# Kernel tuning notes

Hardware: AMD Instinct MI355X
Metric: run time of the kernel (lower is better)

The kernel has to match this reference:

```python
import jax, jax.numpy as jnp
import numpy as np

G = 8        # n_games
D_IN = 128   # per-game state dim
A = 16       # per-game action dim
H1 = 600     # n_hidden_1
H2 = 500     # n_hidden_2
B = 32768    # batch


def setup_inputs() -> dict:
    key = jax.random.key(0)
    ks = jax.random.split(key, 12)
    u = lambda k, shape, bound: jax.random.uniform(k, shape, jnp.float32, -bound, bound)
    state = jax.random.normal(ks[0], (B, D_IN), jnp.float32)
    action = jax.random.normal(ks[1], (B, A), jnp.float32)
    idx = jnp.sort(jax.random.randint(ks[2], (B,), 0, G)).astype(jnp.int32)
    inp = {
        "state": state,
        "action": action,
        "idx": idx,
        # per-game first layer: Linear(D_IN -> H1), uniform(-1/sqrt(fan_in))
        "W1": u(ks[3], (G, H1, D_IN), 1.0 / np.sqrt(D_IN)),
        "b1": u(ks[4], (G, H1), 1.0 / np.sqrt(D_IN)),
        # shared state layer: Linear(H1 -> H2)
        "W2s": u(ks[5], (H2, H1), 1.0 / np.sqrt(H1)),
        "b2s": u(ks[6], (H2,), 1.0 / np.sqrt(H1)),
        # per-game action layer: Linear(A -> H2, bias=False)
        "W2a": u(ks[7], (G, H2, A), 1.0 / np.sqrt(A)),
        # per-game output head: Linear(H2 -> 1), uniform(-0.003, 0.003)
        "W3": u(ks[8], (G, H2), 0.003),
        "b3": u(ks[9], (G,), 0.003),
    }
    return inp


def reference(state, action, idx, W1, b1, W2s, b2s, W2a, W3, b3):
    # Per-game h1 for all games, then pick the routed game per sample.
    # (Reference-clean equivalent of the Python loop over unique idx; idx is
    #  sorted so the original's group reordering is the identity.)
    h1_all = jax.nn.relu(jnp.einsum('bd,ghd->bgh', state, W1) + b1)      # [B,G,H1]
    h1 = jnp.take_along_axis(h1_all, idx[:, None, None], axis=1)[:, 0]  # [B,H1]

    h2a_all = jnp.einsum('ba,gha->bgh', action, W2a)                     # [B,G,H2]
    h2a = jnp.take_along_axis(h2a_all, idx[:, None, None], axis=1)[:, 0]

    h2 = jnp.einsum('bh,kh->bk', h1, W2s) + b2s + h2a                    # [B,H2]
    h_f = jax.nn.relu(h2)  # features == 'relu'

    q_all = jnp.einsum('bh,gh->bg', h_f, W3) + b3                        # [B,G]
    q = jnp.take_along_axis(q_all, idx[:, None], axis=1)[:, 0]           # [B]
    return q
```

## Files before the change

### kernel.cpp

```cpp
#include <hip/hip_runtime.h>

#define G_ 8
#define DIN 128
#define ACT 16
#define H1 600
#define H2 500
#define H1P 608
#define H2P 512
#define BT 128
#define NBLK 256
#define NCHUNK 19
#define NTHR 512

#define OFF_W2S 0
#define OFF_W1  622592
#define OFF_W2A 1867776
#define OFF_B1  1998848
#define OFF_B2S 2018304
#define OFF_W3  2020352
#define PREP_BYTES 2036736

#define LDS_H1  0u
#define LDS_W1  16384u
#define LDS_B1  32768u
#define LDS_IDX 52224u
#define LDS_RED 52736u
#define LDS_TOTAL 56832

typedef __attribute__((ext_vector_type(8))) short short8;
typedef __attribute__((ext_vector_type(4))) float f32x4;
typedef __attribute__((ext_vector_type(16))) float f32x16;

__device__ __forceinline__ unsigned short f2bf(float f) {
  unsigned u = __float_as_uint(f);
  unsigned r = u + 0x7fffu + ((u >> 16) & 1u);
  return (unsigned short)(r >> 16);
}

__device__ __forceinline__ short8 pack8(const float* v) {
  short8 p;
#pragma unroll
  for (int j = 0; j < 8; ++j) p[j] = (short)f2bf(v[j]);
  return p;
}

__device__ __forceinline__ unsigned long long pack4(f32x4 v) {
  unsigned long long pk = 0;
#pragma unroll
  for (int j = 0; j < 4; ++j)
    pk |= (unsigned long long)f2bf(v[j]) << (16 * j);
  return pk;
}

__device__ __forceinline__ void stage1k(unsigned lds_off, const void* g) {
  __builtin_amdgcn_global_load_lds(
      (const __attribute__((address_space(1))) unsigned int*)(unsigned long long)g,
      (__attribute__((address_space(3))) unsigned int*)lds_off,
      16, 0, 0);
}

__global__ __launch_bounds__(256) void prep_kernel(
    const float* __restrict__ W1, const float* __restrict__ b1,
    const float* __restrict__ W2s, const float* __restrict__ b2s,
    const float* __restrict__ W2a, const float* __restrict__ W3,
    char* __restrict__ ws)
{
  unsigned long long* w2s_img = (unsigned long long*)(ws + OFF_W2S);
  unsigned long long* w1_img  = (unsigned long long*)(ws + OFF_W1);
  unsigned long long* w2a_img = (unsigned long long*)(ws + OFF_W2A);
  float* b1p  = (float*)(ws + OFF_B1);
  float* b2sp = (float*)(ws + OFF_B2S);
  float* w3p  = (float*)(ws + OFF_W3);
  const int tid = blockIdx.x * blockDim.x + threadIdx.x;
  const int nthr = gridDim.x * blockDim.x;

  for (int u = tid; u < 75000; u += nthr) {
    const int e0 = u * 4;
    const int c = e0 / 600, k0 = e0 - c * 600;
    f32x4 v = *(const f32x4*)(W2s + e0);
    const int chunk = k0 >> 5, t = (k0 >> 4) & 1, khi = (k0 >> 3) & 1, j0 = k0 & 7;
    const int l = (c & 31) + khi * 32, ct = c >> 5;
    const int base = ((chunk * 2 + t) * 16 + ct) * 64 + l;
    w2s_img[base * 2 + (j0 >> 2)] = pack4(v);
  }
  for (int u = tid; u < 153600; u += nthr) {
    const int e0 = u * 4;
    const int g = e0 / 76800;
    const int rem = e0 - g * 76800;
    const int f = rem >> 7, d0 = rem & 127;
    f32x4 v = *(const f32x4*)(W1 + e0);
    const int chunk = f >> 5, ft = (f >> 4) & 1, fl = f & 15;
    const int ks = d0 >> 5, lhi = (d0 >> 3) & 3, j0 = d0 & 7;
    const int base = ((g * NCHUNK + chunk) * 8 + ks * 2 + ft) * 64 + (lhi * 16 + fl);
    w1_img[base * 2 + (j0 >> 2)] = pack4(v);
  }
  for (int u = tid; u < 16000; u += nthr) {
    const int e0 = u * 4;
    const int g = e0 / 8000;
    const int rem = e0 - g * 8000;
    const int c = rem >> 4, a0 = rem & 15;
    f32x4 v = *(const f32x4*)(W2a + e0);
    const int khi = (a0 >> 3) & 1, j0 = a0 & 7;
    const int l = (c & 31) + khi * 32, ct = c >> 5;
    const int base = (g * 16 + ct) * 64 + l;
    w2a_img[base * 2 + (j0 >> 2)] = pack4(v);
  }
  for (int e = tid; e < G_ * H1; e += nthr) {
    const int g = e / H1, f = e - g * H1;
    b1p[g * H1P + f] = b1[e];
  }
  for (int e = tid; e < H2; e += nthr) b2sp[e] = b2s[e];
  for (int e = tid; e < G_ * H2; e += nthr) {
    const int g = e / H2, c = e - g * H2;
    w3p[g * H2P + c] = W3[e];
  }
}

__global__ __launch_bounds__(NTHR, 2) void critic_fused(
    const float* __restrict__ state, const float* __restrict__ action,
    const int* __restrict__ idx, const float* __restrict__ b3,
    const char* __restrict__ ws, float* __restrict__ out)
{
  extern __shared__ char smem[];
  const int tid = threadIdx.x, lane = tid & 63, w = tid >> 6;
  const int s0 = blockIdx.x * BT;
  int* idx_lds = (int*)(smem + LDS_IDX);
  float* b1lds = (float*)(smem + LDS_B1);
  float* red   = (float*)(smem + LDS_RED);

  const unsigned short* w2simg = (const unsigned short*)(ws + OFF_W2S);
  const unsigned short* w1img  = (const unsigned short*)(ws + OFF_W1);
  const unsigned short* w2aimg = (const unsigned short*)(ws + OFF_W2A);
  const float* b1p  = (const float*)(ws + OFF_B1);
  const float* b2sp = (const float*)(ws + OFF_B2S);
  const float* w3p  = (const float*)(ws + OFF_W3);

  if (tid < BT) idx_lds[tid] = idx[s0 + tid];
  for (int u = tid; u < (G_ * H1P) / 4; u += NTHR)
    ((f32x4*)b1lds)[u] = ((const f32x4*)b1p)[u];
  __syncthreads();
  const int g_lo = idx_lds[0], g_hi = idx_lds[BT - 1];
  const int myg  = idx_lds[w * 16 + (lane & 15)];

  short8 bs[4];
  {
    const float* sp = state + (size_t)(s0 + w * 16 + (lane & 15)) * DIN + ((lane >> 4) << 3);
#pragma unroll
    for (int ks = 0; ks < 4; ++ks) {
      float v[8];
      f32x4 t0 = *(const f32x4*)(sp + ks * 32), t1 = *(const f32x4*)(sp + ks * 32 + 4);
      v[0]=t0[0];v[1]=t0[1];v[2]=t0[2];v[3]=t0[3];
      v[4]=t1[0];v[5]=t1[1];v[6]=t1[2];v[7]=t1[3];
      bs[ks] = pack8(v);
    }
  }
  short8 bact[4];
#pragma unroll
  for (int nt = 0; nt < 4; ++nt) {
    const float* ap = action + (size_t)(s0 + nt * 32 + (lane & 31)) * ACT + ((lane >> 5) << 3);
    float v[8];
    f32x4 a0 = *(const f32x4*)ap, a1 = *(const f32x4*)(ap + 4);
    v[0]=a0[0];v[1]=a0[1];v[2]=a0[2];v[3]=a0[3];
    v[4]=a1[0];v[5]=a1[1];v[6]=a1[2];v[7]=a1[3];
    bact[nt] = pack8(v);
  }

  const char* w1src = (const char*)(ws + OFF_W1) + (size_t)g_lo * NCHUNK * 8192;
  stage1k(LDS_W1 + (unsigned)(tid * 16), w1src + tid * 16);
  stage1k(LDS_W1 + (unsigned)(8192 + tid * 16), w1src + 8192 + tid * 16);

  short8 afc[2][2], afn[2][2];
#pragma unroll
  for (int t = 0; t < 2; ++t)
#pragma unroll
    for (int cti = 0; cti < 2; ++cti)
      afc[t][cti] = *(const short8*)(w2simg + ((((size_t)0 * 2 + t) * 16 + w * 2 + cti) * 64 + lane) * 8);

  f32x16 acc[2][4];
#pragma unroll
  for (int a = 0; a < 2; ++a)
#pragma unroll
    for (int n = 0; n < 4; ++n)
#pragma unroll
      for (int r = 0; r < 16; ++r) acc[a][n][r] = 0.f;
  for (int g = g_lo; g <= g_hi; ++g) {
#pragma unroll
    for (int cti = 0; cti < 2; ++cti) {
      short8 af = *(const short8*)(w2aimg + (((size_t)g * 16 + w * 2 + cti) * 64 + lane) * 8);
#pragma unroll
      for (int nt = 0; nt < 4; ++nt) {
        f32x16 z;
#pragma unroll
        for (int r = 0; r < 16; ++r) z[r] = 0.f;
        f32x16 t = __builtin_amdgcn_mfma_f32_32x32x16_bf16(af, bact[nt], z, 0, 0, 0);
        const bool p = (idx_lds[nt * 32 + (lane & 31)] == g);
#pragma unroll
        for (int r = 0; r < 16; ++r) acc[cti][nt][r] = p ? t[r] : acc[cti][nt][r];
      }
    }
  }

  auto produce = [&](int c, int buf) {
    f32x4 kept[2];
#pragma unroll
    for (int f = 0; f < 2; ++f) { kept[f][0]=0.f;kept[f][1]=0.f;kept[f][2]=0.f;kept[f][3]=0.f; }
    for (int g = g_lo; g <= g_hi; ++g) {
      f32x4 a1[2];
#pragma unroll
      for (int f = 0; f < 2; ++f) { a1[f][0]=0.f;a1[f][1]=0.f;a1[f][2]=0.f;a1[f][3]=0.f; }
#pragma unroll
      for (int ks = 0; ks < 4; ++ks)
#pragma unroll
        for (int ft = 0; ft < 2; ++ft) {
          short8 aw;
          if (g == g_lo)
            aw = *(const short8*)(smem + LDS_W1 + (unsigned)(buf * 8192 + ((ks * 2 + ft) * 64 + lane) * 16));
          else
            aw = *(const short8*)(w1img + (((size_t)(g * NCHUNK + c) * 8 + ks * 2 + ft) * 64 + lane) * 8);
          a1[ft] = __builtin_amdgcn_mfma_f32_16x16x32_bf16(aw, bs[ks], a1[ft], 0, 0, 0);
        }
      if (myg == g) { kept[0] = a1[0]; kept[1] = a1[1]; }
    }
    const int kloc = (lane >> 4) << 2, khalf = lane >> 5;
    const int nt = w >> 1, s32 = (w & 1) * 16 + (lane & 15);
#pragma unroll
    for (int ft = 0; ft < 2; ++ft) {
      const int f0 = c * 32 + ft * 16 + kloc;
      f32x4 bv = *(const f32x4*)(b1lds + myg * H1P + f0);
      unsigned long long pk = 0;
#pragma unroll
      for (int r = 0; r < 4; ++r) {
        float hv = fmaxf(kept[ft][r] + bv[r], 0.f);
        pk |= (unsigned long long)f2bf(hv) << (16 * r);
      }
      *(unsigned long long*)(smem + LDS_H1 + (unsigned)(buf * 8192 +
          (ft * 4 + nt) * 1024 + (khalf * 32 + s32) * 16 + (kloc & 7) * 2)) = pk;
    }
  };

  asm volatile("s_waitcnt vmcnt(0)" ::: "memory");
  __builtin_amdgcn_sched_barrier(0);
  produce(0, 0);
  asm volatile("s_waitcnt lgkmcnt(0)" ::: "memory");
  __builtin_amdgcn_sched_barrier(0);
  __builtin_amdgcn_s_barrier();

  for (int i = 0; i < NCHUNK; ++i) {
    const int cur = i & 1;
    if (i + 2 < NCHUNK)
      stage1k(LDS_W1 + (unsigned)(cur * 8192 + tid * 16),
              w1src + (size_t)(i + 2) * 8192 + tid * 16);
    if (i + 1 < NCHUNK) {
#pragma unroll
      for (int t = 0; t < 2; ++t)
#pragma unroll
        for (int cti = 0; cti < 2; ++cti)
          afn[t][cti] = *(const short8*)(w2simg + ((((size_t)(i + 1) * 2 + t) * 16 + w * 2 + cti) * 64 + lane) * 8);
    }
    short8 bf[2][4];
#pragma unroll
    for (int t = 0; t < 2; ++t)
#pragma unroll
      for (int nt = 0; nt < 4; ++nt)
        bf[t][nt] = *(const short8*)(smem + LDS_H1 + (unsigned)(cur * 8192 + ((t * 4 + nt) * 64 + lane) * 16));
    __builtin_amdgcn_s_setprio(1);
#pragma unroll
    for (int t = 0; t < 2; ++t)
#pragma unroll
      for (int cti = 0; cti < 2; ++cti)
#pragma unroll
        for (int nt = 0; nt < 4; ++nt)
          acc[cti][nt] = __builtin_amdgcn_mfma_f32_32x32x16_bf16(afc[t][cti], bf[t][nt], acc[cti][nt], 0, 0, 0);
    __builtin_amdgcn_s_setprio(0);
    if (i + 1 < NCHUNK) {
      if (i + 2 < NCHUNK) { asm volatile("s_waitcnt vmcnt(5)" ::: "memory"); }
      else                { asm volatile("s_waitcnt vmcnt(4)" ::: "memory"); }
      __builtin_amdgcn_sched_barrier(0);
      produce(i + 1, cur ^ 1);
    }
    asm volatile("s_waitcnt lgkmcnt(0)" ::: "memory");
    __builtin_amdgcn_sched_barrier(0);
    __builtin_amdgcn_s_barrier();
#pragma unroll
    for (int t = 0; t < 2; ++t)
#pragma unroll
      for (int cti = 0; cti < 2; ++cti)
        afc[t][cti] = afn[t][cti];
  }

  float qp[4] = {0.f, 0.f, 0.f, 0.f};
  int gs[4];
#pragma unroll
  for (int nt = 0; nt < 4; ++nt) gs[nt] = idx_lds[nt * 32 + (lane & 31)];
#pragma unroll
  for (int cti = 0; cti < 2; ++cti) {
    const int cbase = (w * 2 + cti) * 32 + ((lane >> 5) << 2);
#pragma unroll
    for (int r = 0; r < 16; ++r) {
      const int c = cbase + (r & 3) + ((r >> 2) << 3);
      const float b2v = b2sp[c];
#pragma unroll
      for (int nt = 0; nt < 4; ++nt) {
        float v2 = fmaxf(acc[cti][nt][r] + b2v, 0.f);
        qp[nt] += v2 * w3p[gs[nt] * H2P + c];
      }
    }
  }
#pragma unroll
  for (int nt = 0; nt < 4; ++nt) {
    float v = qp[nt] + __shfl_xor(qp[nt], 32, 64);
    if (lane < 32) red[w * BT + nt * 32 + lane] = v;
  }
  __syncthreads();
  if (tid < BT) {
    float s = 0.f;
#pragma unroll
    for (int ww = 0; ww < 8; ++ww) s += red[ww * BT + tid];
    out[s0 + tid] = s + b3[idx_lds[tid]];
  }
}

extern "C" void kernel_launch(void* const* d_in, const int* in_sizes, int n_in,
                              void* d_out, int out_size, void* d_ws, size_t ws_size,
                              hipStream_t stream) {
  const float* state  = (const float*)d_in[0];
  const float* action = (const float*)d_in[1];
  const int*   idx    = (const int*)d_in[2];
  const float* W1     = (const float*)d_in[3];
  const float* b1     = (const float*)d_in[4];
  const float* W2s    = (const float*)d_in[5];
  const float* b2s    = (const float*)d_in[6];
  const float* W2a    = (const float*)d_in[7];
  const float* W3     = (const float*)d_in[8];
  const float* b3     = (const float*)d_in[9];
  float* out = (float*)d_out;
  char* ws = (char*)d_ws;

  hipMemsetAsync(ws, 0, PREP_BYTES, stream);
  hipLaunchKernelGGL(prep_kernel, dim3(1024), dim3(256), 0, stream,
                     W1, b1, W2s, b2s, W2a, W3, ws);
  hipLaunchKernelGGL(critic_fused, dim3(NBLK), dim3(NTHR), LDS_TOTAL, stream,
                     state, action, idx, b3, ws, out);
}
```

Measured before the change: 126.3 us.

## Deepen W1 LDS pipeline to four chunks, stage both game sides, drop memset

Rewrites the main loop to process two chunks per phase. It uses a four-deep ring of W1 and h1 LDS buffers, and stages W1 for both the low and high game into LDS instead of reading the second game straight from global memory. The prep kernel now writes zero padding itself, which removes the hipMemsetAsync, and b1 is staged into LDS asynchronously. LDS use grows to about 125 KB, which likely allows only one block per CU instead of the two declared in launch bounds. The chunk-pairing index logic near the tail looks delicate.

```diff
diff --git a/kernel.cpp b/kernel.cpp
--- a/kernel.cpp
+++ b/kernel.cpp
@@ -5,27 +5,27 @@
 #define ACT 16
 #define H1 600
 #define H2 500
-#define H1P 608
 #define H2P 512
+#define B1S 768
 #define BT 128
 #define NBLK 256
 #define NCHUNK 19
+#define NPHASE 9
 #define NTHR 512
 
 #define OFF_W2S 0
 #define OFF_W1  622592
 #define OFF_W2A 1867776
 #define OFF_B1  1998848
-#define OFF_B2S 2018304
-#define OFF_W3  2020352
-#define PREP_BYTES 2036736
+#define OFF_B2S 2023424
+#define OFF_W3  2025472
 
 #define LDS_H1  0u
-#define LDS_W1  16384u
-#define LDS_B1  32768u
-#define LDS_IDX 52224u
-#define LDS_RED 52736u
-#define LDS_TOTAL 56832
+#define LDS_W1  32768u
+#define LDS_B1  98304u
+#define LDS_IDX 122880u
+#define LDS_RED 123392u
+#define LDS_TOTAL 127488
 
 typedef __attribute__((ext_vector_type(8))) short short8;
 typedef __attribute__((ext_vector_type(4))) float f32x4;
@@ -42,14 +42,6 @@
 #pragma unroll
   for (int j = 0; j < 8; ++j) p[j] = (short)f2bf(v[j]);
   return p;
-}
-
-__device__ __forceinline__ unsigned long long pack4(f32x4 v) {
-  unsigned long long pk = 0;
-#pragma unroll
-  for (int j = 0; j < 4; ++j)
-    pk |= (unsigned long long)f2bf(v[j]) << (16 * j);
-  return pk;
 }
 
 __device__ __forceinline__ void stage1k(unsigned lds_off, const void* g) {
@@ -65,54 +57,85 @@
     const float* __restrict__ W2a, const float* __restrict__ W3,
     char* __restrict__ ws)
 {
-  unsigned long long* w2s_img = (unsigned long long*)(ws + OFF_W2S);
-  unsigned long long* w1_img  = (unsigned long long*)(ws + OFF_W1);
-  unsigned long long* w2a_img = (unsigned long long*)(ws + OFF_W2A);
-  float* b1p  = (float*)(ws + OFF_B1);
-  float* b2sp = (float*)(ws + OFF_B2S);
-  float* w3p  = (float*)(ws + OFF_W3);
+  short8* w2s_img = (short8*)(ws + OFF_W2S);
+  short8* w1_img  = (short8*)(ws + OFF_W1);
+  short8* w2a_img = (short8*)(ws + OFF_W2A);
+  f32x4* b1p  = (f32x4*)(ws + OFF_B1);
+  f32x4* b2sp = (f32x4*)(ws + OFF_B2S);
+  f32x4* w3p  = (f32x4*)(ws + OFF_W3);
   const int tid = blockIdx.x * blockDim.x + threadIdx.x;
   const int nthr = gridDim.x * blockDim.x;
 
-  for (int u = tid; u < 75000; u += nthr) {
-    const int e0 = u * 4;
-    const int c = e0 / 600, k0 = e0 - c * 600;
-    f32x4 v = *(const f32x4*)(W2s + e0);
-    const int chunk = k0 >> 5, t = (k0 >> 4) & 1, khi = (k0 >> 3) & 1, j0 = k0 & 7;
-    const int l = (c & 31) + khi * 32, ct = c >> 5;
-    const int base = ((chunk * 2 + t) * 16 + ct) * 64 + l;
-    w2s_img[base * 2 + (j0 >> 2)] = pack4(v);
-  }
-  for (int u = tid; u < 153600; u += nthr) {
-    const int e0 = u * 4;
-    const int g = e0 / 76800;
-    const int rem = e0 - g * 76800;
-    const int f = rem >> 7, d0 = rem & 127;
-    f32x4 v = *(const f32x4*)(W1 + e0);
-    const int chunk = f >> 5, ft = (f >> 4) & 1, fl = f & 15;
-    const int ks = d0 >> 5, lhi = (d0 >> 3) & 3, j0 = d0 & 7;
-    const int base = ((g * NCHUNK + chunk) * 8 + ks * 2 + ft) * 64 + (lhi * 16 + fl);
-    w1_img[base * 2 + (j0 >> 2)] = pack4(v);
-  }
-  for (int u = tid; u < 16000; u += nthr) {
-    const int e0 = u * 4;
-    const int g = e0 / 8000;
-    const int rem = e0 - g * 8000;
-    const int c = rem >> 4, a0 = rem & 15;
-    f32x4 v = *(const f32x4*)(W2a + e0);
-    const int khi = (a0 >> 3) & 1, j0 = a0 & 7;
-    const int l = (c & 31) + khi * 32, ct = c >> 5;
-    const int base = (g * 16 + ct) * 64 + l;
-    w2a_img[base * 2 + (j0 >> 2)] = pack4(v);
-  }
-  for (int e = tid; e < G_ * H1; e += nthr) {
-    const int g = e / H1, f = e - g * H1;
-    b1p[g * H1P + f] = b1[e];
-  }
-  for (int e = tid; e < H2; e += nthr) b2sp[e] = b2s[e];
-  for (int e = tid; e < G_ * H2; e += nthr) {
-    const int g = e / H2, c = e - g * H2;
-    w3p[g * H2P + c] = W3[e];
+  for (int s = tid; s < 38912; s += nthr) {
+    const int chunk = s >> 11, t = (s >> 10) & 1, ct = (s >> 6) & 15, l = s & 63;
+    const int c  = ct * 32 + (l & 31);
+    const int k0 = chunk * 32 + t * 16 + ((l >> 5) << 3);
+    float v[8];
+    if (c < H2 && k0 < H1) {
+      const float* p = W2s + (size_t)c * H1 + k0;
+      f32x4 a0 = *(const f32x4*)p, a1 = *(const f32x4*)(p + 4);
+      v[0]=a0[0];v[1]=a0[1];v[2]=a0[2];v[3]=a0[3];
+      v[4]=a1[0];v[5]=a1[1];v[6]=a1[2];v[7]=a1[3];
+    } else {
+#pragma unroll
+      for (int j = 0; j < 8; ++j) v[j] = 0.f;
+    }
+    w2s_img[s] = pack8(v);
+  }
+  for (int s = tid; s < 77824; s += nthr) {
+    const int g = s / 9728, r = s - g * 9728;
+    const int chunk = r >> 9, r2 = r & 511;
+    const int ks = r2 >> 7, ft = (r2 >> 6) & 1, l = r2 & 63;
+    const int f  = chunk * 32 + ft * 16 + (l & 15);
+    const int d0 = ks * 32 + ((l >> 4) << 3);
+    float v[8];
+    if (f < H1) {
+      const float* p = W1 + ((size_t)g * H1 + f) * DIN + d0;
+      f32x4 a0 = *(const f32x4*)p, a1 = *(const f32x4*)(p + 4);
+      v[0]=a0[0];v[1]=a0[1];v[2]=a0[2];v[3]=a0[3];
+      v[4]=a1[0];v[5]=a1[1];v[6]=a1[2];v[7]=a1[3];
+    } else {
+#pragma unroll
+      for (int j = 0; j < 8; ++j) v[j] = 0.f;
+    }
+    w1_img[s] = pack8(v);
+  }
+  for (int s = tid; s < 8192; s += nthr) {
+    const int g = s >> 10, ct = (s >> 6) & 15, l = s & 63;
+    const int c  = ct * 32 + (l & 31);
+    const int a0 = (l >> 5) << 3;
+    float v[8];
+    if (c < H2) {
+      const float* p = W2a + ((size_t)g * H2 + c) * ACT + a0;
+      f32x4 x0 = *(const f32x4*)p, x1 = *(const f32x4*)(p + 4);
+      v[0]=x0[0];v[1]=x0[1];v[2]=x0[2];v[3]=x0[3];
+      v[4]=x1[0];v[5]=x1[1];v[6]=x1[2];v[7]=x1[3];
+    } else {
+#pragma unroll
+      for (int j = 0; j < 8; ++j) v[j] = 0.f;
+    }
+    w2a_img[s] = pack8(v);
+  }
+  for (int s = tid; s < 1536; s += nthr) {
+    const int g = s / 192, f0 = (s - g * 192) * 4;
+    f32x4 v;
+    if (f0 < H1) v = *(const f32x4*)(b1 + g * H1 + f0);
+    else { v[0]=0.f;v[1]=0.f;v[2]=0.f;v[3]=0.f; }
+    b1p[s] = v;
+  }
+  for (int s = tid; s < 128; s += nthr) {
+    const int c0 = s * 4;
+    f32x4 v;
+    if (c0 < H2) v = *(const f32x4*)(b2s + c0);
+    else { v[0]=0.f;v[1]=0.f;v[2]=0.f;v[3]=0.f; }
+    b2sp[s] = v;
+  }
+  for (int s = tid; s < 1024; s += nthr) {
+    const int g = s >> 7, c0 = (s & 127) * 4;
+    f32x4 v;
+    if (c0 < H2) v = *(const f32x4*)(W3 + g * H2 + c0);
+    else { v[0]=0.f;v[1]=0.f;v[2]=0.f;v[3]=0.f; }
+    w3p[s] = v;
   }
 }
 
@@ -129,18 +152,12 @@
   float* red   = (float*)(smem + LDS_RED);
 
   const unsigned short* w2simg = (const unsigned short*)(ws + OFF_W2S);
-  const unsigned short* w1img  = (const unsigned short*)(ws + OFF_W1);
   const unsigned short* w2aimg = (const unsigned short*)(ws + OFF_W2A);
-  const float* b1p  = (const float*)(ws + OFF_B1);
   const float* b2sp = (const float*)(ws + OFF_B2S);
   const float* w3p  = (const float*)(ws + OFF_W3);
+  const char* w1b   = ws + OFF_W1;
 
   if (tid < BT) idx_lds[tid] = idx[s0 + tid];
-  for (int u = tid; u < (G_ * H1P) / 4; u += NTHR)
-    ((f32x4*)b1lds)[u] = ((const f32x4*)b1p)[u];
-  __syncthreads();
-  const int g_lo = idx_lds[0], g_hi = idx_lds[BT - 1];
-  const int myg  = idx_lds[w * 16 + (lane & 15)];
 
   short8 bs[4];
   {
@@ -164,17 +181,14 @@
     v[4]=a1[0];v[5]=a1[1];v[6]=a1[2];v[7]=a1[3];
     bact[nt] = pack8(v);
   }
-
-  const char* w1src = (const char*)(ws + OFF_W1) + (size_t)g_lo * NCHUNK * 8192;
-  stage1k(LDS_W1 + (unsigned)(tid * 16), w1src + tid * 16);
-  stage1k(LDS_W1 + (unsigned)(8192 + tid * 16), w1src + 8192 + tid * 16);
-
-  short8 afc[2][2], afn[2][2];
-#pragma unroll
-  for (int t = 0; t < 2; ++t)
-#pragma unroll
-    for (int cti = 0; cti < 2; ++cti)
-      afc[t][cti] = *(const short8*)(w2simg + ((((size_t)0 * 2 + t) * 16 + w * 2 + cti) * 64 + lane) * 8);
+#pragma unroll
+  for (int u = 0; u < 3; ++u)
+    stage1k(LDS_B1 + (unsigned)(u * 8192 + tid * 16), ws + OFF_B1 + u * 8192 + tid * 16);
+
+  __syncthreads();
+  const int g_lo = idx_lds[0], g_hi = idx_lds[BT - 1];
+  const int myg  = idx_lds[w * 16 + (lane & 15)];
+  const int nsides = (g_hi > g_lo) ? 2 : 1;
 
   f32x16 acc[2][4];
 #pragma unroll
@@ -199,24 +213,56 @@
       }
     }
   }
-
-  auto produce = [&](int c, int buf) {
+  __builtin_amdgcn_sched_barrier(0);
+
+  auto loadA = [&](int c, short8 af[2][2]) {
+#pragma unroll
+    for (int t = 0; t < 2; ++t)
+#pragma unroll
+      for (int cti = 0; cti < 2; ++cti)
+        af[t][cti] = *(const short8*)(w2simg + ((((size_t)c * 2 + t) * 16 + w * 2 + cti) * 64 + lane) * 8);
+  };
+  auto stageW1 = [&](int c) {
+    const int cs = c > (NCHUNK - 1) ? (NCHUNK - 1) : c;
+    const unsigned bb = (unsigned)((c & 3) * 2);
+    stage1k(LDS_W1 + (bb + 0) * 8192u + (unsigned)(tid * 16),
+            w1b + ((size_t)(g_lo * NCHUNK + cs)) * 8192 + tid * 16);
+    stage1k(LDS_W1 + (bb + 1) * 8192u + (unsigned)(tid * 16),
+            w1b + ((size_t)(g_hi * NCHUNK + cs)) * 8192 + tid * 16);
+  };
+  auto consume = [&](int c, short8 af[2][2]) {
+    short8 bf[2][4];
+    const unsigned hb = LDS_H1 + (unsigned)((c & 3) * 8192);
+#pragma unroll
+    for (int t = 0; t < 2; ++t)
+#pragma unroll
+      for (int nt = 0; nt < 4; ++nt)
+        bf[t][nt] = *(const short8*)(smem + hb + (unsigned)(((t * 4 + nt) * 64 + lane) * 16));
+    __builtin_amdgcn_s_setprio(1);
+#pragma unroll
+    for (int t = 0; t < 2; ++t)
+#pragma unroll
+      for (int cti = 0; cti < 2; ++cti)
+#pragma unroll
+        for (int nt = 0; nt < 4; ++nt)
+          acc[cti][nt] = __builtin_amdgcn_mfma_f32_32x32x16_bf16(af[t][cti], bf[t][nt], acc[cti][nt], 0, 0, 0);
+    __builtin_amdgcn_s_setprio(0);
+  };
+  auto produce = [&](int c) {
     f32x4 kept[2];
 #pragma unroll
     for (int f = 0; f < 2; ++f) { kept[f][0]=0.f;kept[f][1]=0.f;kept[f][2]=0.f;kept[f][3]=0.f; }
-    for (int g = g_lo; g <= g_hi; ++g) {
+    for (int sd = 0; sd < nsides; ++sd) {
+      const int g = sd ? g_hi : g_lo;
       f32x4 a1[2];
 #pragma unroll
       for (int f = 0; f < 2; ++f) { a1[f][0]=0.f;a1[f][1]=0.f;a1[f][2]=0.f;a1[f][3]=0.f; }
+      const unsigned wb = LDS_W1 + (unsigned)(((c & 3) * 2 + sd) * 8192);
 #pragma unroll
       for (int ks = 0; ks < 4; ++ks)
 #pragma unroll
         for (int ft = 0; ft < 2; ++ft) {
-          short8 aw;
-          if (g == g_lo)
-            aw = *(const short8*)(smem + LDS_W1 + (unsigned)(buf * 8192 + ((ks * 2 + ft) * 64 + lane) * 16));
-          else
-            aw = *(const short8*)(w1img + (((size_t)(g * NCHUNK + c) * 8 + ks * 2 + ft) * 64 + lane) * 8);
+          short8 aw = *(const short8*)(smem + wb + (unsigned)(((ks * 2 + ft) * 64 + lane) * 16));
           a1[ft] = __builtin_amdgcn_mfma_f32_16x16x32_bf16(aw, bs[ks], a1[ft], 0, 0, 0);
         }
       if (myg == g) { kept[0] = a1[0]; kept[1] = a1[1]; }
@@ -226,67 +272,50 @@
 #pragma unroll
     for (int ft = 0; ft < 2; ++ft) {
       const int f0 = c * 32 + ft * 16 + kloc;
-      f32x4 bv = *(const f32x4*)(b1lds + myg * H1P + f0);
+      f32x4 bv = *(const f32x4*)(b1lds + myg * B1S + f0);
       unsigned long long pk = 0;
 #pragma unroll
       for (int r = 0; r < 4; ++r) {
         float hv = fmaxf(kept[ft][r] + bv[r], 0.f);
         pk |= (unsigned long long)f2bf(hv) << (16 * r);
       }
-      *(unsigned long long*)(smem + LDS_H1 + (unsigned)(buf * 8192 +
+      *(unsigned long long*)(smem + LDS_H1 + (unsigned)((c & 3) * 8192 +
           (ft * 4 + nt) * 1024 + (khalf * 32 + s32) * 16 + (kloc & 7) * 2)) = pk;
     }
   };
 
-  asm volatile("s_waitcnt vmcnt(0)" ::: "memory");
-  __builtin_amdgcn_sched_barrier(0);
-  produce(0, 0);
+  short8 afA[2][2], afB[2][2];
+  stageW1(0); stageW1(1); stageW1(2); stageW1(3);
+  __builtin_amdgcn_sched_barrier(0);
+  loadA(0, afA);
+  loadA(1, afB);
+  __builtin_amdgcn_sched_barrier(0);
+  asm volatile("s_waitcnt vmcnt(8)" ::: "memory");
+  __builtin_amdgcn_sched_barrier(0);
+  __builtin_amdgcn_s_barrier();
+  produce(0);
+  produce(1);
   asm volatile("s_waitcnt lgkmcnt(0)" ::: "memory");
   __builtin_amdgcn_sched_barrier(0);
   __builtin_amdgcn_s_barrier();
 
-  for (int i = 0; i < NCHUNK; ++i) {
-    const int cur = i & 1;
-    if (i + 2 < NCHUNK)
-      stage1k(LDS_W1 + (unsigned)(cur * 8192 + tid * 16),
-              w1src + (size_t)(i + 2) * 8192 + tid * 16);
-    if (i + 1 < NCHUNK) {
-#pragma unroll
-      for (int t = 0; t < 2; ++t)
-#pragma unroll
-        for (int cti = 0; cti < 2; ++cti)
-          afn[t][cti] = *(const short8*)(w2simg + ((((size_t)(i + 1) * 2 + t) * 16 + w * 2 + cti) * 64 + lane) * 8);
-    }
-    short8 bf[2][4];
-#pragma unroll
-    for (int t = 0; t < 2; ++t)
-#pragma unroll
-      for (int nt = 0; nt < 4; ++nt)
-        bf[t][nt] = *(const short8*)(smem + LDS_H1 + (unsigned)(cur * 8192 + ((t * 4 + nt) * 64 + lane) * 16));
-    __builtin_amdgcn_s_setprio(1);
-#pragma unroll
-    for (int t = 0; t < 2; ++t)
-#pragma unroll
-      for (int cti = 0; cti < 2; ++cti)
-#pragma unroll
-        for (int nt = 0; nt < 4; ++nt)
-          acc[cti][nt] = __builtin_amdgcn_mfma_f32_32x32x16_bf16(afc[t][cti], bf[t][nt], acc[cti][nt], 0, 0, 0);
-    __builtin_amdgcn_s_setprio(0);
-    if (i + 1 < NCHUNK) {
-      if (i + 2 < NCHUNK) { asm volatile("s_waitcnt vmcnt(5)" ::: "memory"); }
-      else                { asm volatile("s_waitcnt vmcnt(4)" ::: "memory"); }
-      __builtin_amdgcn_sched_barrier(0);
-      produce(i + 1, cur ^ 1);
-    }
+  for (int p = 0; p < NPHASE; ++p) {
+    const int c0 = 2 * p, c1 = 2 * p + 1;
+    stageW1(c0 + 4);
+    stageW1(c1 + 4);
+    __builtin_amdgcn_sched_barrier(0);
+    consume(c0, afA);
+    loadA(c0 + 2, afA);
+    consume(c1, afB);
+    loadA(c1 + 3 > NCHUNK - 1 ? NCHUNK - 1 : c1 + 2, afB);
+    produce(c0 + 2);
+    if (p < NPHASE - 1) produce(c1 + 2);
+    asm volatile("s_waitcnt vmcnt(8)" ::: "memory");
     asm volatile("s_waitcnt lgkmcnt(0)" ::: "memory");
     __builtin_amdgcn_sched_barrier(0);
     __builtin_amdgcn_s_barrier();
-#pragma unroll
-    for (int t = 0; t < 2; ++t)
-#pragma unroll
-      for (int cti = 0; cti < 2; ++cti)
-        afc[t][cti] = afn[t][cti];
-  }
+  }
+  consume(NCHUNK - 1, afA);
 
   float qp[4] = {0.f, 0.f, 0.f, 0.f};
   int gs[4];
@@ -336,8 +365,9 @@
   float* out = (float*)d_out;
   char* ws = (char*)d_ws;
 
-  hipMemsetAsync(ws, 0, PREP_BYTES, stream);
-  hipLaunchKernelGGL(prep_kernel, dim3(1024), dim3(256), 0, stream,
+  (void)hipFuncSetAttribute((const void*)critic_fused,
+                            hipFuncAttributeMaxDynamicSharedMemorySize, LDS_TOTAL);
+  hipLaunchKernelGGL(prep_kernel, dim3(2048), dim3(256), 0, stream,
                      W1, b1, W2s, b2s, W2a, W3, ws);
   hipLaunchKernelGGL(critic_fused, dim3(NBLK), dim3(NTHR), LDS_TOTAL, stream,
                      state, action, idx, b3, ws, out);
```

Result: faster. 118.5 us (-6.2%).
